# Kernel optimization log

Measured on AMD Instinct MI355X. Metric: run time of the kernel, lower is better.

## Reference

```python
import jax, jax.numpy as jnp
import numpy as np

NUM_HEADS = 12  # per-branch heads = NUM_HEADS // 3 = 4


def setup_inputs() -> dict:
    key = jax.random.key(0)
    ks = jax.random.split(key, 11)
    B, N, C = 4, 2048, 768
    s = 0.02
    return {
        "x": jax.random.normal(ks[0], (B, N, C), jnp.float32),
        "Wqkv1": jax.random.normal(ks[1], (C, C), jnp.float32) * s,
        "Wqkv2": jax.random.normal(ks[2], (C, C), jnp.float32) * s,
        "Wqkv3": jax.random.normal(ks[3], (C, C), jnp.float32) * s,
        "Wp1": jax.random.normal(ks[4], (C // 3, C), jnp.float32) * s,
        "bp1": jax.random.normal(ks[5], (C,), jnp.float32) * s,
        "Wp2": jax.random.normal(ks[6], (C // 3, C), jnp.float32) * s,
        "bp2": jax.random.normal(ks[7], (C,), jnp.float32) * s,
        "Wp3": jax.random.normal(ks[8], (C // 3, C), jnp.float32) * s,
        "bp3": jax.random.normal(ks[9], (C,), jnp.float32) * s,
        "Wg": jax.random.normal(ks[10], (C, 3), jnp.float32) * s,
    }


def _branch(x, Wqkv, Wp, bp, B, N, C):
    Hb = NUM_HEADS // 3          # heads per branch
    hd = C // NUM_HEADS          # head dim
    scale = hd ** (-0.5)
    qkv = (x @ Wqkv).reshape(B, N, 3, Hb, hd)
    qkv = jnp.transpose(qkv, (2, 0, 3, 1, 4))  # [3, B, Hb, N, hd]
    q, k, v = qkv[0], qkv[1], qkv[2]
    attn = jax.nn.softmax(jnp.einsum('bhqd,bhkd->bhqk', q, k) * scale, axis=-1)
    o = jnp.einsum('bhqk,bhkd->bqhd', attn, v).reshape(B, N, C // 3)
    return o @ Wp + bp  # [B, N, C]


def _gate(z, Wg):
    prob_soft = jax.nn.softmax(z @ Wg, axis=-1)
    prob_hard = jax.nn.one_hot(jnp.argmax(prob_soft, axis=-1), 3, dtype=prob_soft.dtype)
    # straight-through estimator
    return jax.lax.stop_gradient(prob_hard - prob_soft) + prob_soft


def reference(x, Wqkv1, Wqkv2, Wqkv3, Wp1, bp1, Wp2, bp2, Wp3, bp3, Wg):
    B, N, C = x.shape
    prob_true = _gate(x, Wg)                                # [B, N, 3]
    x1 = _branch(x, Wqkv1, Wp1, bp1, B, N, C)
    x2 = _branch(x, Wqkv2, Wp2, bp2, B, N, C)
    x3 = _branch(x, Wqkv3, Wp3, bp3, B, N, C)
    # detached gate path (gate sees stop_gradient(x))
    prob_true_d = _gate(jax.lax.stop_gradient(x), Wg)
    xo = (x1 * prob_true[..., 0:1] + x2 * prob_true[..., 1:2]
          + x3 * prob_true[..., 2:3])
    sg = jax.lax.stop_gradient
    xd = (sg(x1) * prob_true_d[..., 0:1] + sg(x2) * prob_true_d[..., 1:2]
          + sg(x3) * prob_true_d[..., 2:3])
    idx = jnp.argmax(prob_true, axis=-1).reshape(-1, 1)
    return (xo, xd, idx)
```

## Files before the change

kernel.cpp:

```cpp
#include <hip/hip_runtime.h>

typedef short s16x4 __attribute__((ext_vector_type(4)));
typedef short s16x8 __attribute__((ext_vector_type(8)));
typedef float f32x4 __attribute__((ext_vector_type(4)));
typedef unsigned u32x4 __attribute__((ext_vector_type(4)));
typedef unsigned short u16;
typedef unsigned char u8;

__device__ __forceinline__ u16 f2b(float f) {
    union { float f; unsigned u; } v; v.f = f;
    unsigned r = v.u + 0x7FFFu + ((v.u >> 16) & 1u);
    return (u16)(r >> 16);
}

__device__ __forceinline__ float fexp2(float x) {
    float r; asm("v_exp_f32 %0, %1" : "=v"(r) : "v"(x)); return r;
}

__device__ __forceinline__ unsigned cvtpk(float lo, float hi) {
    unsigned r; asm("v_cvt_pk_bf16_f32 %0, %1, %2" : "=v"(r) : "v"(lo), "v"(hi)); return r;
}

__device__ __forceinline__ void GLL(const void* g, void* l) {
    __builtin_amdgcn_global_load_lds(
        (const __attribute__((address_space(1))) unsigned int*)g,
        (__attribute__((address_space(3))) unsigned int*)l, 16, 0, 0);
}

__device__ __forceinline__ void vmwait0() {
    asm volatile("s_waitcnt vmcnt(0)" ::: "memory");
    __builtin_amdgcn_sched_barrier(0);
}

#define QSCALE 0.1803368801111244f

__global__ __launch_bounds__(256) void prolog_kernel(const float* __restrict__ x,
                                                     const float* __restrict__ Wg,
                                                     u16* __restrict__ xb,
                                                     u8* __restrict__ kArr,
                                                     float* __restrict__ out,
                                                     const float* __restrict__ W0,
                                                     const float* __restrict__ W1,
                                                     const float* __restrict__ W2,
                                                     const float* __restrict__ W3,
                                                     const float* __restrict__ W4,
                                                     const float* __restrict__ W5,
                                                     u16* __restrict__ wqt,
                                                     u16* __restrict__ wpt) {
    __shared__ u16 tile[32][34];
    if (blockIdx.x < 2048) {
        int t = blockIdx.x * 4 + (threadIdx.x >> 6);
        int lane = threadIdx.x & 63;
        const float* xr = x + (size_t)t * 768;
        u16* xw = xb + (size_t)t * 768;
        float z0 = 0.f, z1 = 0.f, z2 = 0.f;
        #pragma unroll
        for (int s = 0; s < 3; s++) {
            int base = s * 256 + lane * 4;
            f32x4 v = *(const f32x4*)(xr + base);
            s16x4 o;
            #pragma unroll
            for (int j = 0; j < 4; j++) {
                o[j] = (short)f2b(v[j]);
                z0 = fmaf(v[j], Wg[(base + j) * 3 + 0], z0);
                z1 = fmaf(v[j], Wg[(base + j) * 3 + 1], z1);
                z2 = fmaf(v[j], Wg[(base + j) * 3 + 2], z2);
            }
            *(s16x4*)(xw + base) = o;
        }
        for (int o = 32; o; o >>= 1) {
            z0 += __shfl_xor(z0, o);
            z1 += __shfl_xor(z1, o);
            z2 += __shfl_xor(z2, o);
        }
        if (lane == 0) {
            int k = 0; float b = z0;
            if (z1 > b) { b = z1; k = 1; }
            if (z2 > b) { b = z2; k = 2; }
            out[12582912 + t] = (float)k;
            kArr[t] = (u8)k;
        }
    } else {
        int wb = blockIdx.x - 2048;
        int y, bt;
        if (wb < 1728) { y = wb / 576; bt = wb % 576; }
        else           { int w2 = wb - 1728; y = 3 + w2 / 192; bt = w2 % 192; }
        const float* W; u16* dst; int K;
        if (y < 3) { W = (y == 0) ? W0 : (y == 1) ? W1 : W2; dst = wqt + y * 589824; K = 768; }
        else       { W = (y == 3) ? W3 : (y == 4) ? W4 : W5; dst = wpt + (y - 3) * 196608; K = 256; }
        int ktiles = K >> 5;
        int kt = bt % ktiles, nt = bt / ktiles;
        int tx = threadIdx.x & 31, ty = threadIdx.x >> 5;
        #pragma unroll
        for (int i = 0; i < 4; i++) {
            int k = kt * 32 + ty + i * 8;
            tile[ty + i * 8][tx] = f2b(W[(size_t)k * 768 + nt * 32 + tx]);
        }
        __syncthreads();
        #pragma unroll
        for (int i = 0; i < 4; i++) {
            int n = nt * 32 + ty + i * 8;
            dst[(size_t)n * K + kt * 32 + tx] = tile[tx][ty + i * 8];
        }
    }
}

__global__ __launch_bounds__(64) void compact_kernel(const u8* __restrict__ kArr,
                                                     u16* __restrict__ perm,
                                                     int* __restrict__ cnt,
                                                     int* __restrict__ startA) {
    int batch = blockIdx.x;
    int lane = threadIdx.x;
    const u8* ka = kArr + batch * 2048;
    u16* pm = perm + batch * 2048;
    int off = 0;
    for (int br = 0; br < 3; br++) {
        int c = 0;
        for (int b0 = 0; b0 < 2048; b0 += 64) {
            bool p = (ka[b0 + lane] == (u8)br);
            unsigned long long m = __ballot(p);
            int rank = __popcll(m & ((1ull << lane) - 1ull));
            if (p) pm[off + c + rank] = (u16)(b0 + lane);
            c += __popcll(m);
        }
        if (lane == 0) { cnt[br * 4 + batch] = c; startA[br * 4 + batch] = off; }
        off += c;
    }
}

__global__ __launch_bounds__(256) void qkv_gemm_kernel(const u16* __restrict__ A,
                                                       const u16* __restrict__ Bt_all,
                                                       u16* __restrict__ Qo,
                                                       u16* __restrict__ Ko,
                                                       u16* __restrict__ Vt) {
    __shared__ u16 As[128 * 64];
    __shared__ u16 Bs[128 * 64];
    const int tid = threadIdx.x;
    const int lane = tid & 63, w = tid >> 6, wm = w >> 1, wn = w & 1;
    const int g = lane >> 4, c15 = lane & 15;
    const int cx = c15 & 7;
    const int b = blockIdx.x;
    const int j = b >> 3;
    const int v = j % 18;
    const int branch = v / 6;
    const int m0 = ((b & 7) * 8 + j / 18) * 128;
    const int n0 = (v % 6) * 128;
    const u16* Bt = Bt_all + (size_t)branch * 589824;

    const int l8 = lane >> 3;
    const int ch = (lane & 7) ^ l8;
    const u16* Asrc = A + (size_t)(m0 + w * 32 + l8) * 768 + ch * 8;
    const u16* Bsrc = Bt + (size_t)(n0 + w * 32 + l8) * 768 + ch * 8;
    u16* AsW = As + w * 2048;
    u16* BsW = Bs + w * 2048;

    f32x4 z4 = {0.f, 0.f, 0.f, 0.f};
    f32x4 acc[4][4];
    for (int mi = 0; mi < 4; mi++)
        for (int ni = 0; ni < 4; ni++) acc[mi][ni] = z4;

    for (int k0 = 0; k0 < 768; k0 += 64) {
        __syncthreads();
        #pragma unroll
        for (int it = 0; it < 4; it++) {
            GLL(Asrc + (size_t)(it * 8) * 768 + k0, AsW + it * 512);
            GLL(Bsrc + (size_t)(it * 8) * 768 + k0, BsW + it * 512);
        }
        vmwait0();
        __syncthreads();
        #pragma unroll
        for (int kk = 0; kk < 2; kk++) {
            s16x8 af[4], bf[4];
            #pragma unroll
            for (int i = 0; i < 4; i++) {
                af[i] = *(const s16x8*)&As[(wm * 64 + i * 16 + c15) * 64 + (((kk * 4 + g) ^ cx) * 8)];
                bf[i] = *(const s16x8*)&Bs[(wn * 64 + i * 16 + c15) * 64 + (((kk * 4 + g) ^ cx) * 8)];
            }
            for (int mi = 0; mi < 4; mi++)
                for (int ni = 0; ni < 4; ni++)
                    acc[mi][ni] = __builtin_amdgcn_mfma_f32_16x16x32_bf16(
                        af[mi], bf[ni], acc[mi][ni], 0, 0, 0);
        }
    }

    for (int mi = 0; mi < 4; mi++) {
        int r = m0 + wm * 64 + mi * 16 + g * 4;
        int batch = r >> 11, nbase = r & 2047;
        for (int ni = 0; ni < 4; ni++) {
            int cN = n0 + wn * 64 + ni * 16 + c15;
            int p = cN >> 8, h = (cN >> 6) & 3, d = cN & 63;
            size_t hb = (size_t)((branch * 4 + batch) * 4 + h) * 131072;
            f32x4 vv = acc[mi][ni];
            if (p == 2) {
                s16x4 pk;
                for (int rg = 0; rg < 4; rg++) pk[rg] = (short)f2b(vv[rg]);
                int pos = nbase & 31;
                int slot = ((pos & 15) >> 2) * 8 + ((pos >> 4) << 2);
                *(s16x4*)(Vt + hb + (size_t)d * 2048 + (nbase & ~31) + slot) = pk;
            } else if (p == 0) {
                for (int rg = 0; rg < 4; rg++)
                    Qo[hb + (size_t)(nbase + rg) * 64 + d] = f2b(vv[rg] * QSCALE);
            } else {
                for (int rg = 0; rg < 4; rg++)
                    Ko[hb + (size_t)(nbase + rg) * 64 + d] = f2b(vv[rg]);
            }
        }
    }
}

#define ATTN_STEP(KF, VF) do {                                                              \
    _Pragma("unroll")                                                                       \
    for (int s = 0; s < 2; s++) {                                                           \
        f32x4 sa0 = __builtin_amdgcn_mfma_f32_16x16x32_bf16(KF[0][0], qf[s][0], z4, 0, 0, 0); \
        sa0 = __builtin_amdgcn_mfma_f32_16x16x32_bf16(KF[0][1], qf[s][1], sa0, 0, 0, 0);    \
        f32x4 sa1 = __builtin_amdgcn_mfma_f32_16x16x32_bf16(KF[1][0], qf[s][0], z4, 0, 0, 0); \
        sa1 = __builtin_amdgcn_mfma_f32_16x16x32_bf16(KF[1][1], qf[s][1], sa1, 0, 0, 0);    \
        float q0 = fexp2(sa0[0]), q1 = fexp2(sa0[1]);                                       \
        float q2 = fexp2(sa0[2]), q3 = fexp2(sa0[3]);                                       \
        float q4 = fexp2(sa1[0]), q5 = fexp2(sa1[1]);                                       \
        float q6 = fexp2(sa1[2]), q7 = fexp2(sa1[3]);                                       \
        lsp[s] += ((q0 + q1) + (q2 + q3)) + ((q4 + q5) + (q6 + q7));                        \
        u32x4 pw;                                                                           \
        pw[0] = cvtpk(q0, q1); pw[1] = cvtpk(q2, q3);                                       \
        pw[2] = cvtpk(q4, q5); pw[3] = cvtpk(q6, q7);                                       \
        union { u32x4 w; s16x8 h; } pu; pu.w = pw;                                          \
        s16x8 pb = pu.h;                                                                    \
        _Pragma("unroll")                                                                   \
        for (int dt = 0; dt < 4; dt++)                                                      \
            oac[s][dt] = __builtin_amdgcn_mfma_f32_16x16x32_bf16(VF[dt], pb, oac[s][dt], 0, 0, 0); \
    }                                                                                       \
} while (0)

#define STAGE(B, T) do {                                                  \
    const unsigned char* _ks = Ksrc + (size_t)(T) * 8192;                 \
    const unsigned char* _vs = Vsrc + (size_t)(T) * 128;                  \
    unsigned char* _kd = &lds[(B) * 16384 + w * 2048];                    \
    unsigned char* _vd = &lds[(B) * 16384 + 8192 + w * 2048];             \
    GLL(_ks, _kd); GLL(_ks + 1024, _kd + 1024);                           \
    GLL(_vs, _vd); GLL(_vs + 32768, _vd + 1024);                          \
} while (0)

#define TILE_STEP(B) do {                                                               \
    const unsigned char* _KL = &lds[(B) * 16384];                                       \
    const unsigned char* _VL = &lds[(B) * 16384 + 8192];                                \
    s16x8 kf[2][2], vf[4];                                                              \
    _Pragma("unroll")                                                                   \
    for (int t = 0; t < 2; t++)                                                         \
        _Pragma("unroll")                                                               \
        for (int h = 0; h < 2; h++)                                                     \
            kf[t][h] = *(const s16x8*)(_KL + (t * 16 + c) * 128 + (((h * 4 + g) ^ cx) * 16)); \
    _Pragma("unroll")                                                                   \
    for (int dt = 0; dt < 4; dt++)                                                      \
        vf[dt] = *(const s16x8*)(_VL + (dt * 16 + c) * 128 + ((g ^ cx) * 16));          \
    ATTN_STEP(kf, vf);                                                                  \
    _Pragma("unroll")                                                                   \
    for (int t = 0; t < 2; t++)                                                         \
        _Pragma("unroll")                                                               \
        for (int h = 0; h < 2; h++)                                                     \
            kf[t][h] = *(const s16x8*)(_KL + ((t + 2) * 16 + c) * 128 + (((h * 4 + g) ^ cx) * 16)); \
    _Pragma("unroll")                                                                   \
    for (int dt = 0; dt < 4; dt++)                                                      \
        vf[dt] = *(const s16x8*)(_VL + (dt * 16 + c) * 128 + (((4 + g) ^ cx) * 16));    \
    ATTN_STEP(kf, vf);                                                                  \
} while (0)

__global__ __launch_bounds__(256, 4) void attn_kernel(const u16* __restrict__ Qg,
                                                      const u16* __restrict__ Kg,
                                                      const u16* __restrict__ Vg,
                                                      const u16* __restrict__ perm,
                                                      const int* __restrict__ cnt,
                                                      const int* __restrict__ startA,
                                                      u16* __restrict__ Og) {
    __shared__ unsigned char lds[32768];
    const int tid = threadIdx.x;
    const int w = tid >> 6, lane = tid & 63;
    const int b = blockIdx.x;
    const int j = b >> 3;
    const int inst = (b & 7) * 6 + (j % 6);
    const int branch = inst >> 4, batch = (inst >> 2) & 3, h = inst & 3;
    const int cb = branch * 4 + batch;
    const int count = min(2048, cnt[cb]);
    const int qbase = (j / 6) * 128;
    if (qbase >= count) return;
    const int qt = (j / 6) * 4 + w;
    const int g = lane >> 4, c = lane & 15;
    const int cx = c & 7;
    const u16* ci = perm + batch * 2048 + startA[cb];
    const u16* Qh = Qg + (size_t)inst * 131072;

    const int slot0 = qt * 32 + c, slot1 = slot0 + 16;
    const int n0 = ci[slot0 < count ? slot0 : count - 1] & 2047;
    const int n1 = ci[slot1 < count ? slot1 : count - 1] & 2047;

    f32x4 z4 = {0.f, 0.f, 0.f, 0.f};
    s16x8 qf[2][2];
    #pragma unroll
    for (int kk = 0; kk < 2; kk++) {
        qf[0][kk] = *(const s16x8*)(Qh + (size_t)n0 * 64 + kk * 32 + g * 8);
        qf[1][kk] = *(const s16x8*)(Qh + (size_t)n1 * 64 + kk * 32 + g * 8);
    }

    f32x4 oac[2][4];
    #pragma unroll
    for (int s = 0; s < 2; s++)
        #pragma unroll
        for (int dt = 0; dt < 4; dt++) oac[s][dt] = z4;
    float lsp[2] = {0.f, 0.f};

    const int swz = (((lane & 7) ^ ((lane >> 3) & 7)) << 4);
    const unsigned char* Ksrc = (const unsigned char*)(Kg + (size_t)inst * 131072)
                                + w * 2048 + ((lane >> 3) << 7) + swz;
    const unsigned char* Vsrc = (const unsigned char*)(Vg + (size_t)inst * 131072)
                                + (size_t)w * 65536 + ((lane >> 3) << 12) + swz;

    STAGE(0, 0);
    vmwait0();
    __syncthreads();
    for (int t2 = 0; t2 < 32; t2++) {
        int cur = t2 & 1;
        if (t2 + 1 < 32) STAGE(cur ^ 1, t2 + 1);
        TILE_STEP(cur);
        vmwait0();
        __syncthreads();
    }

    #pragma unroll
    for (int s = 0; s < 2; s++) {
        float ls = lsp[s];
        ls += __shfl_xor(ls, 16);
        ls += __shfl_xor(ls, 32);
        float inv = 1.0f / ls;
        int slot = qt * 32 + s * 16 + c;
        u16* dst = Og + ((size_t)cb * 2048 + slot) * 256 + h * 64;
        #pragma unroll
        for (int dt = 0; dt < 4; dt++) {
            s16x4 ob;
            for (int rg = 0; rg < 4; rg++) ob[rg] = (short)f2b(oac[s][dt][rg] * inv);
            *(s16x4*)(dst + dt * 16 + g * 4) = ob;
        }
    }
}

__global__ __launch_bounds__(256) void proj_gemm_kernel(const u16* __restrict__ Oall,
                                                        const u16* __restrict__ Wpt_all,
                                                        const u16* __restrict__ perm,
                                                        const int* __restrict__ cnt,
                                                        const int* __restrict__ startA,
                                                        const float* __restrict__ bp1,
                                                        const float* __restrict__ bp2,
                                                        const float* __restrict__ bp3,
                                                        float* __restrict__ out) {
    __shared__ u16 As[128 * 64];
    __shared__ u16 Bs[128 * 64];
    const int tid = threadIdx.x;
    const int lane = tid & 63, w = tid >> 6, wm = w >> 1, wn = w & 1;
    const int g = lane >> 4, c15 = lane & 15;
    const int cx = c15 & 7;
    const int branch = blockIdx.z;
    const int m0 = blockIdx.y * 128, n0 = blockIdx.x * 128;
    const int batch = m0 >> 11;
    const int cb = branch * 4 + batch;
    const int count = min(2048, cnt[cb]);
    const int pbase = m0 & 2047;
    if (pbase >= count) return;
    const u16* A = Oall + (size_t)branch * 8192 * 256;
    const u16* Bt = Wpt_all + (size_t)branch * 196608;
    const float* bp = (branch == 0) ? bp1 : ((branch == 1) ? bp2 : bp3);

    const int l8 = lane >> 3;
    const int ch = (lane & 7) ^ l8;
    const u16* Asrc = A + (size_t)(m0 + w * 32 + l8) * 256 + ch * 8;
    const u16* Bsrc = Bt + (size_t)(n0 + w * 32 + l8) * 256 + ch * 8;
    u16* AsW = As + w * 2048;
    u16* BsW = Bs + w * 2048;

    f32x4 z4 = {0.f, 0.f, 0.f, 0.f};
    f32x4 acc[4][4];
    for (int mi = 0; mi < 4; mi++)
        for (int ni = 0; ni < 4; ni++) acc[mi][ni] = z4;

    for (int k0 = 0; k0 < 256; k0 += 64) {
        __syncthreads();
        #pragma unroll
        for (int it = 0; it < 4; it++) {
            GLL(Asrc + (size_t)(it * 8) * 256 + k0, AsW + it * 512);
            GLL(Bsrc + (size_t)(it * 8) * 256 + k0, BsW + it * 512);
        }
        vmwait0();
        __syncthreads();
        #pragma unroll
        for (int kk = 0; kk < 2; kk++) {
            s16x8 af[4], bf[4];
            #pragma unroll
            for (int i = 0; i < 4; i++) {
                af[i] = *(const s16x8*)&As[(wm * 64 + i * 16 + c15) * 64 + (((kk * 4 + g) ^ cx) * 8)];
                bf[i] = *(const s16x8*)&Bs[(wn * 64 + i * 16 + c15) * 64 + (((kk * 4 + g) ^ cx) * 8)];
            }
            for (int mi = 0; mi < 4; mi++)
                for (int ni = 0; ni < 4; ni++)
                    acc[mi][ni] = __builtin_amdgcn_mfma_f32_16x16x32_bf16(
                        af[mi], bf[ni], acc[mi][ni], 0, 0, 0);
        }
    }

    const u16* ci = perm + batch * 2048 + startA[cb];
    for (int mi = 0; mi < 4; mi++) {
        int r = pbase + wm * 64 + mi * 16 + g * 4;
        for (int ni = 0; ni < 4; ni++) {
            int cN = n0 + wn * 64 + ni * 16 + c15;
            float bj = bp[cN];
            f32x4 v = acc[mi][ni];
            for (int rg = 0; rg < 4; rg++) {
                int slot = r + rg;
                if (slot < count) {
                    int t = batch * 2048 + (ci[slot] & 2047);
                    float wv = v[rg] + bj;
                    out[(size_t)t * 768 + cN] = wv;
                    out[6291456u + (size_t)t * 768 + cN] = wv;
                }
            }
        }
    }
}

extern "C" void kernel_launch(void* const* d_in, const int* in_sizes, int n_in,
                              void* d_out, int out_size, void* d_ws, size_t ws_size,
                              hipStream_t stream) {
    const float* x   = (const float*)d_in[0];
    const float* Wq1 = (const float*)d_in[1];
    const float* Wq2 = (const float*)d_in[2];
    const float* Wq3 = (const float*)d_in[3];
    const float* Wp1 = (const float*)d_in[4];
    const float* bp1 = (const float*)d_in[5];
    const float* Wp2 = (const float*)d_in[6];
    const float* bp2 = (const float*)d_in[7];
    const float* Wp3 = (const float*)d_in[8];
    const float* bp3 = (const float*)d_in[9];
    const float* Wg  = (const float*)d_in[10];
    float* out = (float*)d_out;

    char* ws = (char*)d_ws;
    u16* xb    = (u16*)(ws + 0);
    u16* wqt   = (u16*)(ws + 12582912);
    u16* wpt   = (u16*)(ws + 16121856);
    u16* Qb    = (u16*)(ws + 17301504);
    u16* Kb    = (u16*)(ws + 29884416);
    u16* Vtb   = (u16*)(ws + 42467328);
    u16* Ob    = (u16*)(ws + 55050240);
    u16* perm  = (u16*)(ws + 67633152);
    int* cnt   = (int*)(ws + 67649536);
    int* start = (int*)(ws + 67649600);
    u8*  kArr  = (u8*) (ws + 67649664);

    prolog_kernel<<<4352, 256, 0, stream>>>(x, Wg, xb, kArr, out,
                                            Wq1, Wq2, Wq3, Wp1, Wp2, Wp3, wqt, wpt);
    compact_kernel<<<4, 64, 0, stream>>>(kArr, perm, cnt, start);
    qkv_gemm_kernel<<<1152, 256, 0, stream>>>(xb, wqt, Qb, Kb, Vtb);
    attn_kernel<<<768, 256, 0, stream>>>(Qb, Kb, Vtb, perm, cnt, start, Ob);
    proj_gemm_kernel<<<dim3(6, 64, 3), 256, 0, stream>>>(Ob, wpt, perm, cnt, start, bp1, bp2, bp3, out);
}
```

Before: 135.2 us.

## Double-buffer LDS tiles in QKV GEMM to overlap loads with MFMA

The QKV projection GEMM now keeps two LDS buffers for the A and B tiles. It issues the global-to-LDS loads for the next K-step before running the MFMA compute on the current buffer, and drops one barrier per iteration. The aim is to hide global load latency behind matrix math. In exchange the kernel uses twice the LDS (64KB per block), which may lower occupancy.

```diff
diff --git a/kernel.cpp b/kernel.cpp
--- a/kernel.cpp
+++ b/kernel.cpp
@@ -128,13 +128,37 @@
     }
 }
 
+#define QKV_STAGE(BUF, K0) do {                                                     \
+    _Pragma("unroll")                                                               \
+    for (int it = 0; it < 4; it++) {                                                \
+        GLL(Asrc + (size_t)(it * 8) * 768 + (K0), &As[BUF][w * 2048 + it * 512]);   \
+        GLL(Bsrc + (size_t)(it * 8) * 768 + (K0), &Bs[BUF][w * 2048 + it * 512]);   \
+    }                                                                               \
+} while (0)
+
+#define QKV_COMPUTE(BUF) do {                                                                     \
+    _Pragma("unroll")                                                                             \
+    for (int kk = 0; kk < 2; kk++) {                                                              \
+        s16x8 af[4], bf[4];                                                                       \
+        _Pragma("unroll")                                                                         \
+        for (int i = 0; i < 4; i++) {                                                             \
+            af[i] = *(const s16x8*)&As[BUF][(wm * 64 + i * 16 + c15) * 64 + (((kk * 4 + g) ^ cx) * 8)]; \
+            bf[i] = *(const s16x8*)&Bs[BUF][(wn * 64 + i * 16 + c15) * 64 + (((kk * 4 + g) ^ cx) * 8)]; \
+        }                                                                                         \
+        for (int mi = 0; mi < 4; mi++)                                                            \
+            for (int ni = 0; ni < 4; ni++)                                                        \
+                acc[mi][ni] = __builtin_amdgcn_mfma_f32_16x16x32_bf16(                            \
+                    af[mi], bf[ni], acc[mi][ni], 0, 0, 0);                                        \
+    }                                                                                             \
+} while (0)
+
 __global__ __launch_bounds__(256) void qkv_gemm_kernel(const u16* __restrict__ A,
                                                        const u16* __restrict__ Bt_all,
                                                        u16* __restrict__ Qo,
                                                        u16* __restrict__ Ko,
                                                        u16* __restrict__ Vt) {
-    __shared__ u16 As[128 * 64];
-    __shared__ u16 Bs[128 * 64];
+    __shared__ u16 As[2][128 * 64];
+    __shared__ u16 Bs[2][128 * 64];
     const int tid = threadIdx.x;
     const int lane = tid & 63, w = tid >> 6, wm = w >> 1, wn = w & 1;
     const int g = lane >> 4, c15 = lane & 15;
@@ -151,36 +175,21 @@
     const int ch = (lane & 7) ^ l8;
     const u16* Asrc = A + (size_t)(m0 + w * 32 + l8) * 768 + ch * 8;
     const u16* Bsrc = Bt + (size_t)(n0 + w * 32 + l8) * 768 + ch * 8;
-    u16* AsW = As + w * 2048;
-    u16* BsW = Bs + w * 2048;
 
     f32x4 z4 = {0.f, 0.f, 0.f, 0.f};
     f32x4 acc[4][4];
     for (int mi = 0; mi < 4; mi++)
         for (int ni = 0; ni < 4; ni++) acc[mi][ni] = z4;
 
-    for (int k0 = 0; k0 < 768; k0 += 64) {
-        __syncthreads();
-        #pragma unroll
-        for (int it = 0; it < 4; it++) {
-            GLL(Asrc + (size_t)(it * 8) * 768 + k0, AsW + it * 512);
-            GLL(Bsrc + (size_t)(it * 8) * 768 + k0, BsW + it * 512);
-        }
+    QKV_STAGE(0, 0);
+    vmwait0();
+    __syncthreads();
+    for (int st = 0; st < 12; st++) {
+        int cur = st & 1;
+        if (st + 1 < 12) QKV_STAGE(cur ^ 1, (st + 1) * 64);
+        QKV_COMPUTE(cur);
         vmwait0();
         __syncthreads();
-        #pragma unroll
-        for (int kk = 0; kk < 2; kk++) {
-            s16x8 af[4], bf[4];
-            #pragma unroll
-            for (int i = 0; i < 4; i++) {
-                af[i] = *(const s16x8*)&As[(wm * 64 + i * 16 + c15) * 64 + (((kk * 4 + g) ^ cx) * 8)];
-                bf[i] = *(const s16x8*)&Bs[(wn * 64 + i * 16 + c15) * 64 + (((kk * 4 + g) ^ cx) * 8)];
-            }
-            for (int mi = 0; mi < 4; mi++)
-                for (int ni = 0; ni < 4; ni++)
-                    acc[mi][ni] = __builtin_amdgcn_mfma_f32_16x16x32_bf16(
-                        af[mi], bf[ni], acc[mi][ni], 0, 0, 0);
-        }
     }
 
     for (int mi = 0; mi < 4; mi++) {
```

Result: slower. 140.4 us (+3.8%).

## Compute Q only for routed tokens in QKV GEMM, gathering rows via permutation

Applied to the files above, without the earlier changes.

The QKV GEMM now gathers A rows through the per-branch token permutation for the Q columns (n0<256) and returns early for tiles past the routed count. Q is therefore stored in compacted order, so attention indexes it directly without an indirect lookup. This skips Q projection work for tokens not routed to a branch and simplifies attention's Q load. The compact kernel also preloads its routing bytes into registers with an unrolled loop. The cost is scattered row gathers in the GEMM A loads and a dependency of the GEMM on the compaction output.

```diff
diff --git a/kernel.cpp b/kernel.cpp
--- a/kernel.cpp
+++ b/kernel.cpp
@@ -112,15 +112,19 @@
     int batch = blockIdx.x;
     int lane = threadIdx.x;
     const u8* ka = kArr + batch * 2048;
+    u8 kv[32];
+    #pragma unroll
+    for (int i = 0; i < 32; i++) kv[i] = ka[i * 64 + lane];
     u16* pm = perm + batch * 2048;
     int off = 0;
     for (int br = 0; br < 3; br++) {
         int c = 0;
-        for (int b0 = 0; b0 < 2048; b0 += 64) {
-            bool p = (ka[b0 + lane] == (u8)br);
+        #pragma unroll
+        for (int i = 0; i < 32; i++) {
+            bool p = (kv[i] == (u8)br);
             unsigned long long m = __ballot(p);
             int rank = __popcll(m & ((1ull << lane) - 1ull));
-            if (p) pm[off + c + rank] = (u16)(b0 + lane);
+            if (p) pm[off + c + rank] = (u16)(i * 64 + lane);
             c += __popcll(m);
         }
         if (lane == 0) { cnt[br * 4 + batch] = c; startA[br * 4 + batch] = off; }
@@ -130,6 +134,9 @@
 
 __global__ __launch_bounds__(256) void qkv_gemm_kernel(const u16* __restrict__ A,
                                                        const u16* __restrict__ Bt_all,
+                                                       const u16* __restrict__ perm,
+                                                       const int* __restrict__ cnt,
+                                                       const int* __restrict__ startA,
                                                        u16* __restrict__ Qo,
                                                        u16* __restrict__ Ko,
                                                        u16* __restrict__ Vt) {
@@ -149,7 +156,24 @@
 
     const int l8 = lane >> 3;
     const int ch = (lane & 7) ^ l8;
-    const u16* Asrc = A + (size_t)(m0 + w * 32 + l8) * 768 + ch * 8;
+    const int batch0 = m0 >> 11, pbase = m0 & 2047;
+    const u16* Arow[4];
+    if (n0 < 256) {
+        const int cb = branch * 4 + batch0;
+        const int count = min(2048, cnt[cb]);
+        if (pbase >= count) return;
+        const u16* ci = perm + batch0 * 2048 + startA[cb];
+        #pragma unroll
+        for (int it = 0; it < 4; it++) {
+            int slot = pbase + w * 32 + l8 + it * 8;
+            int tok = ci[slot < count ? slot : count - 1] & 2047;
+            Arow[it] = A + (size_t)(batch0 * 2048 + tok) * 768 + ch * 8;
+        }
+    } else {
+        #pragma unroll
+        for (int it = 0; it < 4; it++)
+            Arow[it] = A + (size_t)(m0 + w * 32 + l8 + it * 8) * 768 + ch * 8;
+    }
     const u16* Bsrc = Bt + (size_t)(n0 + w * 32 + l8) * 768 + ch * 8;
     u16* AsW = As + w * 2048;
     u16* BsW = Bs + w * 2048;
@@ -163,7 +187,7 @@
         __syncthreads();
         #pragma unroll
         for (int it = 0; it < 4; it++) {
-            GLL(Asrc + (size_t)(it * 8) * 768 + k0, AsW + it * 512);
+            GLL(Arow[it] + k0, AsW + it * 512);
             GLL(Bsrc + (size_t)(it * 8) * 768 + k0, BsW + it * 512);
         }
         vmwait0();
@@ -267,9 +291,7 @@
 __global__ __launch_bounds__(256, 4) void attn_kernel(const u16* __restrict__ Qg,
                                                       const u16* __restrict__ Kg,
                                                       const u16* __restrict__ Vg,
-                                                      const u16* __restrict__ perm,
                                                       const int* __restrict__ cnt,
-                                                      const int* __restrict__ startA,
                                                       u16* __restrict__ Og) {
     __shared__ unsigned char lds[32768];
     const int tid = threadIdx.x;
@@ -285,19 +307,14 @@
     const int qt = (j / 6) * 4 + w;
     const int g = lane >> 4, c = lane & 15;
     const int cx = c & 7;
-    const u16* ci = perm + batch * 2048 + startA[cb];
     const u16* Qh = Qg + (size_t)inst * 131072;
-
-    const int slot0 = qt * 32 + c, slot1 = slot0 + 16;
-    const int n0 = ci[slot0 < count ? slot0 : count - 1] & 2047;
-    const int n1 = ci[slot1 < count ? slot1 : count - 1] & 2047;
 
     f32x4 z4 = {0.f, 0.f, 0.f, 0.f};
     s16x8 qf[2][2];
     #pragma unroll
     for (int kk = 0; kk < 2; kk++) {
-        qf[0][kk] = *(const s16x8*)(Qh + (size_t)n0 * 64 + kk * 32 + g * 8);
-        qf[1][kk] = *(const s16x8*)(Qh + (size_t)n1 * 64 + kk * 32 + g * 8);
+        qf[0][kk] = *(const s16x8*)(Qh + (size_t)(qt * 32 + c) * 64 + kk * 32 + g * 8);
+        qf[1][kk] = *(const s16x8*)(Qh + (size_t)(qt * 32 + 16 + c) * 64 + kk * 32 + g * 8);
     }
 
     f32x4 oac[2][4];
@@ -455,7 +472,7 @@
     prolog_kernel<<<4352, 256, 0, stream>>>(x, Wg, xb, kArr, out,
                                             Wq1, Wq2, Wq3, Wp1, Wp2, Wp3, wqt, wpt);
     compact_kernel<<<4, 64, 0, stream>>>(kArr, perm, cnt, start);
-    qkv_gemm_kernel<<<1152, 256, 0, stream>>>(xb, wqt, Qb, Kb, Vtb);
-    attn_kernel<<<768, 256, 0, stream>>>(Qb, Kb, Vtb, perm, cnt, start, Ob);
+    qkv_gemm_kernel<<<1152, 256, 0, stream>>>(xb, wqt, perm, cnt, start, Qb, Kb, Vtb);
+    attn_kernel<<<768, 256, 0, stream>>>(Qb, Kb, Vtb, cnt, Ob);
     proj_gemm_kernel<<<dim3(6, 64, 3), 256, 0, stream>>>(Ob, wpt, perm, cnt, start, bp1, bp2, bp3, out);
 }
```

Result: faster. 124.8 us (-7.7%).
